# Kernel tuning notes

Hardware: AMD Instinct MI355X
Metric: run time of the kernel (lower is better)

## Reference

```python
import jax, jax.numpy as jnp
import numpy as np

B, S, D = 2048, 8, 1280
K = 1                 # n_components_remove
HIGH_T = 0.6          # PC1_HIGH_ACTIVITY_THRESHOLD
STORM_T = 0.8         # solar_storm_threshold


def setup_inputs() -> dict:
    key = jax.random.key(0)
    k1, k2 = jax.random.split(key, 2)
    features = jax.random.normal(k1, (B, S, D), dtype=jnp.float32)
    kp_index = jax.random.uniform(k2, (B,), dtype=jnp.float32) * 9.0
    cmr_gate = jnp.ones((1,), dtype=jnp.float32)  # nn.Parameter(torch.ones(1))
    return {"features": features, "kp_index": kp_index, "cmr_gate": cmr_gate}


def reference(features, kp_index, cmr_gate):
    # Per-sample standardization over the feature axis (numpy std, ddof=0)
    mu = features.mean(axis=2, keepdims=True)            # (B, S, 1)
    sigma = features.std(axis=2, keepdims=True) + 1e-8   # (B, S, 1)
    fn = (features - mu) / sigma                         # (B, S, D)

    # Batched thin SVD of the (S, D) normalized feature matrix
    U, sv, Vt = jnp.linalg.svd(fn, full_matrices=False)  # (B,S,S), (B,S), (B,S,D)
    var = sv * sv
    pc1_ratio = var[:, 0] / (var.sum(axis=-1) + 1e-8)    # (B,)

    # solar_flag: 0 normal, 1 high activity, 2 storm
    solar_flag = (pc1_ratio >= HIGH_T).astype(jnp.int32) + (pc1_ratio >= STORM_T).astype(jnp.int32)

    # Rank-K reconstruction of the common-mode (solar) component
    low = jnp.einsum('bsk,bk,bkd->bsd', U[:, :, :K], sv[:, :K], Vt[:, :K, :])
    clean = (fn - low) * sigma + mu                      # de-normalized cleaned features

    # Kp-gating: amplify CMR when Kp >= 5
    kp_gate = 1.0 + 0.5 * (kp_index >= 5.0).astype(features.dtype)[:, None, None]
    clean = features + kp_gate * (clean - features)

    # Learnable gate
    gate = jax.nn.sigmoid(cmr_gate)[0]
    features_clean = features + gate * (clean - features)
    return features_clean, pc1_ratio, solar_flag
```

## Files before the change

kernel.cpp:

```cpp
#include <hip/hip_runtime.h>
#include <math.h>


#define SV 8
#define DV 1280
#define D4 320
#define BSTRIDE (SV*DV)
#define LDW 44
#define NP 44
#define WSS 17

__global__ __launch_bounds__(320)
void cmr_gram(const float* __restrict__ feat,
              float* __restrict__ gram)
{
    __shared__ float lds[NP * LDW];
    const int tid  = threadIdx.x;
    const int lane = tid & 63;
    const int wq   = tid >> 6;
    const int b    = blockIdx.x;

    const float4* __restrict__ f4 = (const float4*)(feat + (size_t)b * BSTRIDE);
    const int d4 = wq * 64 + lane;
    float4 f[8];
#pragma unroll
    for (int s = 0; s < 8; ++s) f[s] = f4[s * D4 + d4];

    float Sr[8], C[36];
#pragma unroll
    for (int s = 0; s < 8; ++s) Sr[s] = (f[s].x + f[s].y) + (f[s].z + f[s].w);
    {
        int idx = 0;
#pragma unroll
        for (int i2 = 0; i2 < 8; ++i2)
#pragma unroll
            for (int j2 = i2; j2 < 8; ++j2) {
                float t0 = fmaf(f[i2].x, f[j2].x, fmaf(f[i2].y, f[j2].y, 0.f));
                C[idx] = fmaf(f[i2].z, f[j2].z, fmaf(f[i2].w, f[j2].w, t0));
                ++idx;
            }
    }
#pragma unroll
    for (int m = 1; m <= 4; m <<= 1) {
#pragma unroll
        for (int s = 0; s < 8; ++s) Sr[s] += __shfl_xor(Sr[s], m);
#pragma unroll
        for (int t = 0; t < 36; ++t) C[t] += __shfl_xor(C[t], m);
    }
    {
        const int p = wq * 8 + (lane >> 3);
        if ((lane & 7) == 0) {
#pragma unroll
            for (int t = 0; t < 36; ++t) lds[t * LDW + p] = C[t];
#pragma unroll
            for (int s = 0; s < 8; ++s) lds[(36 + s) * LDW + p] = Sr[s];
        }
    }
    __syncthreads();
    if (wq != 0) return;

    if (lane < NP) {
        const float4* l4 = (const float4*)lds;
        float4 a4 = make_float4(0.f, 0.f, 0.f, 0.f);
#pragma unroll
        for (int q = 0; q < 10; ++q) {
            float4 v = l4[lane * (LDW / 4) + q];
            a4.x += v.x; a4.y += v.y; a4.z += v.z; a4.w += v.w;
        }
        gram[(size_t)b * NP + lane] = (a4.x + a4.y) + (a4.z + a4.w);
    }
}

__global__ __launch_bounds__(256)
void cmr_eigen(const float* __restrict__ gram,
               const float* __restrict__ kp,
               const float* __restrict__ cmr_gate,
               float* __restrict__ coef,
               float* __restrict__ out,
               int Bn)
{
    const int lane = threadIdx.x & 63;
    const int b = blockIdx.x * 4 + (threadIdx.x >> 6);

    const int Lr = (lane < NP) ? lane : 0;
    const float tot = gram[(size_t)b * NP + Lr];

    const int i = lane >> 3, j = lane & 7;
    const int a_ = (i < j) ? i : j;
    const int b_ = (i < j) ? j : i;
    const int tii = 8 * i - (i * (i - 1)) / 2;
    const int tjj = 8 * j - (j * (j - 1)) / 2;
    const int tij = 8 * a_ - (a_ * (a_ - 1)) / 2 + (b_ - a_);
    const float Cij = __shfl(tot, tij);
    const float Ci  = __shfl(tot, tii);
    const float Cj  = __shfl(tot, tjj);
    const float Si  = __shfl(tot, 36 + i);
    const float Sj  = __shfl(tot, 36 + j);

    const float invD = 1.f / (float)DV;
    const float mui = Si * invD, muj = Sj * invD;
    const float vari = fmaxf(Ci * invD - mui * mui, 0.f);
    const float varj = fmaxf(Cj * invD - muj * muj, 0.f);
    const float sigi  = sqrtf(vari) + 1e-8f;
    const float rsigi = 1.f / sigi;
    const float rsigj = 1.f / (sqrtf(varj) + 1e-8f);
    const float G = ((Cij - (float)DV * mui * muj) * rsigi) * rsigj;

    float tr = 0.f;
#pragma unroll
    for (int k = 0; k < 8; ++k) tr += __shfl(G, 9 * k);

    float A = G / fmaxf(tr, 1e-30f);
#pragma unroll
    for (int t = 0; t < 14; ++t) {
        float nb = 0.f;
#pragma unroll
        for (int k = 0; k < 8; ++k)
            nb = fmaf(__shfl(A, i * 8 + k), __shfl(A, k * 8 + j), nb);
        float dg = 0.f;
#pragma unroll
        for (int k = 0; k < 8; ++k) dg += __shfl(nb, 9 * k);
        A = nb / fmaxf(dg, 1e-30f);
    }
    float best = __shfl(A, 0); int bj = 0;
#pragma unroll
    for (int k = 1; k < 8; ++k) {
        float dk = __shfl(A, 9 * k);
        if (dk > best) { best = dk; bj = k; }
    }
    float u = __shfl(A, i * 8 + bj);
    {
        float nn = 0.f;
#pragma unroll
        for (int k = 0; k < 8; ++k) nn += __shfl(u * u, 9 * k);
        u *= rsqrtf(fmaxf(nn, 1e-30f));
    }
#pragma unroll
    for (int it = 0; it < 2; ++it) {
        float y = G * __shfl(u, 9 * j);
#pragma unroll
        for (int m = 1; m <= 4; m <<= 1) y += __shfl_xor(y, m);
        float ny = 0.f;
#pragma unroll
        for (int k = 0; k < 8; ++k) ny += __shfl(y * y, 9 * k);
        u = y * rsqrtf(fmaxf(ny, 1e-30f));
    }
    float v = G * u * __shfl(u, 9 * j);
#pragma unroll
    for (int m = 1; m <= 4; m <<= 1) v += __shfl_xor(v, m);
    float lam = 0.f;
#pragma unroll
    for (int k = 0; k < 8; ++k) lam += __shfl(v, 9 * k);
    const float pc1 = lam / (tr + 1e-8f);

    const float gate = 1.f / (1.f + expf(-cmr_gate[0]));
    const float kpg  = (kp[b] >= 5.0f) ? 1.5f : 1.0f;
    const float Gt   = gate * kpg;

    float bc = 0.f;
#pragma unroll
    for (int k = 0; k < 8; ++k) bc += __shfl(u * rsigi * mui, 9 * k);

    float* wsb = coef + (size_t)b * WSS;
    if (j == 0) {
        wsb[i]     = u * rsigi;
        wsb[8 + i] = Gt * sigi * u;
    }
    if (lane == 0) {
        wsb[16] = bc;
        out[(size_t)Bn * BSTRIDE + b] = pc1;
        const float flag = (pc1 >= 0.6f ? 1.f : 0.f) + (pc1 >= 0.8f ? 1.f : 0.f);
        out[(size_t)Bn * BSTRIDE + Bn + b] = flag;
    }
}

__global__ __launch_bounds__(320)
void cmr_apply(const float* __restrict__ feat,
               const float* __restrict__ coef,
               float* __restrict__ out)
{
    const int tid  = threadIdx.x;
    const int lane = tid & 63;
    const int wq   = tid >> 6;
    const int b    = blockIdx.x;

    const float* __restrict__ wsb = coef + (size_t)b * WSS;
    float a[8], c[8];
#pragma unroll
    for (int s = 0; s < 8; ++s) { a[s] = wsb[s]; c[s] = wsb[8 + s]; }
    const float bc = wsb[16];

    const float4* __restrict__ f4 = (const float4*)(feat + (size_t)b * BSTRIDE);
    float4* __restrict__ o4 = (float4*)(out + (size_t)b * BSTRIDE);
    const int d4 = wq * 64 + lane;

    float4 f[8];
#pragma unroll
    for (int s = 0; s < 8; ++s) f[s] = f4[s * D4 + d4];

    float4 p = make_float4(-bc, -bc, -bc, -bc);
#pragma unroll
    for (int s = 0; s < 8; ++s) {
        p.x = fmaf(a[s], f[s].x, p.x);
        p.y = fmaf(a[s], f[s].y, p.y);
        p.z = fmaf(a[s], f[s].z, p.z);
        p.w = fmaf(a[s], f[s].w, p.w);
    }
#pragma unroll
    for (int s = 0; s < 8; ++s) {
        float4 o;
        o.x = fmaf(-c[s], p.x, f[s].x);
        o.y = fmaf(-c[s], p.y, f[s].y);
        o.z = fmaf(-c[s], p.z, f[s].z);
        o.w = fmaf(-c[s], p.w, f[s].w);
        o4[s * D4 + d4] = o;
    }
}

extern "C" void kernel_launch(void* const* d_in, const int* in_sizes, int n_in,
                              void* d_out, int out_size, void* d_ws, size_t ws_size,
                              hipStream_t stream) {
    const float* feat = (const float*)d_in[0];
    const float* kp   = (const float*)d_in[1];
    const float* gate = (const float*)d_in[2];
    float* out = (float*)d_out;
    const int Bn = in_sizes[0] / BSTRIDE;

    float* gram = (float*)d_ws;
    float* coef = gram + (size_t)Bn * NP;

    cmr_gram <<<Bn,      320, 0, stream>>>(feat, gram);
    cmr_eigen<<<Bn / 4,  256, 0, stream>>>(gram, kp, gate, coef, out, Bn);
    cmr_apply<<<Bn,      320, 0, stream>>>(feat, coef, out);
}
```

Baseline: 178.5 us.

## Compute Gram matrix with bf16 split MFMA and run eigen solve per thread

The Gram/sum reduction now runs on MFMA matrix cores: each fp32 value is split into bf16 hi and lo parts, and hi*hi, hi*lo and sums against a ones vector are accumulated. Each wave handles two batch items. The eigen kernel is reorganized so each thread owns one batch item with the full 8x8 matrix in registers, replacing cross-lane shuffles. It also cuts the squaring iterations from 14 to 12 and uses symmetric products. This trades exact fp32 accumulation for split-bf16 precision (the lo*lo term is dropped) and raises register pressure in the eigen kernel.

Result: faster. 174.5 us (-2.2%).

```diff
diff --git a/kernel.cpp b/kernel.cpp
--- a/kernel.cpp
+++ b/kernel.cpp
@@ -6,72 +6,82 @@
 #define DV 1280
 #define D4 320
 #define BSTRIDE (SV*DV)
-#define LDW 44
-#define NP 44
+#define GSZ 136
 #define WSS 17
 
-__global__ __launch_bounds__(320)
-void cmr_gram(const float* __restrict__ feat,
-              float* __restrict__ gram)
+typedef __attribute__((ext_vector_type(8))) short bf16x8;
+typedef __attribute__((ext_vector_type(4))) float f32x4;
+
+union BF8 { bf16x8 v; short s[8]; };
+
+__device__ __forceinline__ short f2bf(float x) {
+    unsigned u = __float_as_uint(x);
+    return (short)((u + 0x7FFFu + ((u >> 16) & 1u)) >> 16);
+}
+__device__ __forceinline__ float bf2f(short h) {
+    return __uint_as_float(((unsigned)(unsigned short)h) << 16);
+}
+
+__global__ __launch_bounds__(256)
+void cmr_gram(const float* __restrict__ feat, float* __restrict__ gram)
 {
-    __shared__ float lds[NP * LDW];
-    const int tid  = threadIdx.x;
-    const int lane = tid & 63;
-    const int wq   = tid >> 6;
-    const int b    = blockIdx.x;
-
-    const float4* __restrict__ f4 = (const float4*)(feat + (size_t)b * BSTRIDE);
-    const int d4 = wq * 64 + lane;
-    float4 f[8];
-#pragma unroll
-    for (int s = 0; s < 8; ++s) f[s] = f4[s * D4 + d4];
-
-    float Sr[8], C[36];
-#pragma unroll
-    for (int s = 0; s < 8; ++s) Sr[s] = (f[s].x + f[s].y) + (f[s].z + f[s].w);
-    {
-        int idx = 0;
-#pragma unroll
-        for (int i2 = 0; i2 < 8; ++i2)
-#pragma unroll
-            for (int j2 = i2; j2 < 8; ++j2) {
-                float t0 = fmaf(f[i2].x, f[j2].x, fmaf(f[i2].y, f[j2].y, 0.f));
-                C[idx] = fmaf(f[i2].z, f[j2].z, fmaf(f[i2].w, f[j2].w, t0));
-                ++idx;
-            }
-    }
-#pragma unroll
-    for (int m = 1; m <= 4; m <<= 1) {
-#pragma unroll
-        for (int s = 0; s < 8; ++s) Sr[s] += __shfl_xor(Sr[s], m);
-#pragma unroll
-        for (int t = 0; t < 36; ++t) C[t] += __shfl_xor(C[t], m);
-    }
-    {
-        const int p = wq * 8 + (lane >> 3);
-        if ((lane & 7) == 0) {
-#pragma unroll
-            for (int t = 0; t < 36; ++t) lds[t * LDW + p] = C[t];
-#pragma unroll
-            for (int s = 0; s < 8; ++s) lds[(36 + s) * LDW + p] = Sr[s];
-        }
-    }
-    __syncthreads();
-    if (wq != 0) return;
-
-    if (lane < NP) {
-        const float4* l4 = (const float4*)lds;
-        float4 a4 = make_float4(0.f, 0.f, 0.f, 0.f);
-#pragma unroll
-        for (int q = 0; q < 10; ++q) {
-            float4 v = l4[lane * (LDW / 4) + q];
-            a4.x += v.x; a4.y += v.y; a4.z += v.z; a4.w += v.w;
-        }
-        gram[(size_t)b * NP + lane] = (a4.x + a4.y) + (a4.z + a4.w);
-    }
-}
-
-__global__ __launch_bounds__(256)
+    const int lane = threadIdx.x & 63;
+    const int wid  = (blockIdx.x * 256 + threadIdx.x) >> 6;
+    const int m    = lane & 15;
+    const int quad = lane >> 4;
+    const int bt   = m >> 3;
+    const int row  = m & 7;
+
+    const float* __restrict__ fb =
+        feat + ((size_t)(wid * 2 + bt)) * BSTRIDE + (size_t)row * DV;
+
+    BF8 ones;
+#pragma unroll
+    for (int j = 0; j < 8; ++j) ones.s[j] = (short)0x3F80;
+
+    f32x4 accHH = {0.f, 0.f, 0.f, 0.f};
+    f32x4 accHL = {0.f, 0.f, 0.f, 0.f};
+    f32x4 accS  = {0.f, 0.f, 0.f, 0.f};
+
+#pragma unroll 4
+    for (int c = 0; c < 40; ++c) {
+        const int k0 = c * 32 + quad * 8;
+        const float4 x0 = *(const float4*)(fb + k0);
+        const float4 x1 = *(const float4*)(fb + k0 + 4);
+        float x[8] = {x0.x, x0.y, x0.z, x0.w, x1.x, x1.y, x1.z, x1.w};
+        BF8 hi, lo;
+#pragma unroll
+        for (int j = 0; j < 8; ++j) {
+            hi.s[j] = f2bf(x[j]);
+            lo.s[j] = f2bf(x[j] - bf2f(hi.s[j]));
+        }
+        accHH = __builtin_amdgcn_mfma_f32_16x16x32_bf16(hi.v, hi.v,   accHH, 0, 0, 0);
+        accHL = __builtin_amdgcn_mfma_f32_16x16x32_bf16(hi.v, lo.v,   accHL, 0, 0, 0);
+        accS  = __builtin_amdgcn_mfma_f32_16x16x32_bf16(hi.v, ones.v, accS,  0, 0, 0);
+        accS  = __builtin_amdgcn_mfma_f32_16x16x32_bf16(lo.v, ones.v, accS,  0, 0, 0);
+    }
+
+    const int colb = (lane & 15) >> 3;
+    const int col  = lane & 7;
+#pragma unroll
+    for (int r = 0; r < 4; ++r) {
+        const int rowg = quad * 4 + r;
+        if ((rowg >> 3) == colb) {
+            float* gb = gram + ((size_t)(wid * 2 + colb)) * GSZ;
+            gb[(rowg & 7) * 8 + col]      = accHH[r];
+            gb[64 + (rowg & 7) * 8 + col] = accHL[r];
+        }
+    }
+    if ((lane & 15) == 0) {
+#pragma unroll
+        for (int r = 0; r < 4; ++r) {
+            const int rowg = quad * 4 + r;
+            gram[((size_t)(wid * 2 + (rowg >> 3))) * GSZ + 128 + (rowg & 7)] = accS[r];
+        }
+    }
+}
+
+__global__ __launch_bounds__(64, 1)
 void cmr_eigen(const float* __restrict__ gram,
                const float* __restrict__ kp,
                const float* __restrict__ cmr_gate,
@@ -79,78 +89,109 @@
                float* __restrict__ out,
                int Bn)
 {
-    const int lane = threadIdx.x & 63;
-    const int b = blockIdx.x * 4 + (threadIdx.x >> 6);
-
-    const int Lr = (lane < NP) ? lane : 0;
-    const float tot = gram[(size_t)b * NP + Lr];
-
-    const int i = lane >> 3, j = lane & 7;
-    const int a_ = (i < j) ? i : j;
-    const int b_ = (i < j) ? j : i;
-    const int tii = 8 * i - (i * (i - 1)) / 2;
-    const int tjj = 8 * j - (j * (j - 1)) / 2;
-    const int tij = 8 * a_ - (a_ * (a_ - 1)) / 2 + (b_ - a_);
-    const float Cij = __shfl(tot, tij);
-    const float Ci  = __shfl(tot, tii);
-    const float Cj  = __shfl(tot, tjj);
-    const float Si  = __shfl(tot, 36 + i);
-    const float Sj  = __shfl(tot, 36 + j);
-
+    const int b = blockIdx.x * 64 + threadIdx.x;
+    const float* __restrict__ g = gram + (size_t)b * GSZ;
+
+    float G[8][8], S[8], mu[8], sig[8], rsig[8];
+#pragma unroll
+    for (int i = 0; i < 8; ++i) {
+#pragma unroll
+        for (int j = 0; j < 8; ++j)
+            G[i][j] = g[i * 8 + j] + g[64 + i * 8 + j] + g[64 + j * 8 + i];
+        S[i] = g[128 + i];
+    }
     const float invD = 1.f / (float)DV;
-    const float mui = Si * invD, muj = Sj * invD;
-    const float vari = fmaxf(Ci * invD - mui * mui, 0.f);
-    const float varj = fmaxf(Cj * invD - muj * muj, 0.f);
-    const float sigi  = sqrtf(vari) + 1e-8f;
-    const float rsigi = 1.f / sigi;
-    const float rsigj = 1.f / (sqrtf(varj) + 1e-8f);
-    const float G = ((Cij - (float)DV * mui * muj) * rsigi) * rsigj;
+#pragma unroll
+    for (int i = 0; i < 8; ++i) {
+        mu[i] = S[i] * invD;
+        const float var = fmaxf(G[i][i] * invD - mu[i] * mu[i], 0.f);
+        sig[i]  = sqrtf(var) + 1e-8f;
+        rsig[i] = 1.f / sig[i];
+    }
+#pragma unroll
+    for (int i = 0; i < 8; ++i)
+#pragma unroll
+        for (int j = 0; j < 8; ++j)
+            G[i][j] = (G[i][j] - (float)DV * mu[i] * mu[j]) * rsig[i] * rsig[j];
 
     float tr = 0.f;
 #pragma unroll
-    for (int k = 0; k < 8; ++k) tr += __shfl(G, 9 * k);
-
-    float A = G / fmaxf(tr, 1e-30f);
-#pragma unroll
-    for (int t = 0; t < 14; ++t) {
-        float nb = 0.f;
-#pragma unroll
-        for (int k = 0; k < 8; ++k)
-            nb = fmaf(__shfl(A, i * 8 + k), __shfl(A, k * 8 + j), nb);
-        float dg = 0.f;
-#pragma unroll
-        for (int k = 0; k < 8; ++k) dg += __shfl(nb, 9 * k);
-        A = nb / fmaxf(dg, 1e-30f);
-    }
-    float best = __shfl(A, 0); int bj = 0;
-#pragma unroll
-    for (int k = 1; k < 8; ++k) {
-        float dk = __shfl(A, 9 * k);
-        if (dk > best) { best = dk; bj = k; }
-    }
-    float u = __shfl(A, i * 8 + bj);
+    for (int i = 0; i < 8; ++i) tr += G[i][i];
+
+    float A[8][8];
+    {
+        const float rt = 1.f / fmaxf(tr, 1e-30f);
+#pragma unroll
+        for (int i = 0; i < 8; ++i)
+#pragma unroll
+            for (int j = 0; j < 8; ++j) A[i][j] = G[i][j] * rt;
+    }
+#pragma unroll
+    for (int t = 0; t < 12; ++t) {
+        float Bm[8][8];
+        float trB = 0.f;
+#pragma unroll
+        for (int i = 0; i < 8; ++i)
+#pragma unroll
+            for (int j = i; j < 8; ++j) {
+                float acc = 0.f;
+#pragma unroll
+                for (int k = 0; k < 8; ++k)
+                    acc = fmaf(A[i][k], A[j][k], acc);
+                Bm[i][j] = acc;
+                if (i == j) trB += acc;
+            }
+        const float rt = 1.f / fmaxf(trB, 1e-30f);
+#pragma unroll
+        for (int i = 0; i < 8; ++i)
+#pragma unroll
+            for (int j = i; j < 8; ++j) {
+                const float v = Bm[i][j] * rt;
+                A[i][j] = v; A[j][i] = v;
+            }
+    }
+    int bj = 0; float best = A[0][0];
+#pragma unroll
+    for (int k = 1; k < 8; ++k)
+        if (A[k][k] > best) { best = A[k][k]; bj = k; }
+    float u[8];
+#pragma unroll
+    for (int i = 0; i < 8; ++i) {
+        float v = A[i][0];
+#pragma unroll
+        for (int k = 1; k < 8; ++k) v = (bj == k) ? A[i][k] : v;
+        u[i] = v;
+    }
     {
         float nn = 0.f;
 #pragma unroll
-        for (int k = 0; k < 8; ++k) nn += __shfl(u * u, 9 * k);
-        u *= rsqrtf(fmaxf(nn, 1e-30f));
+        for (int i = 0; i < 8; ++i) nn = fmaf(u[i], u[i], nn);
+        const float r = rsqrtf(fmaxf(nn, 1e-30f));
+#pragma unroll
+        for (int i = 0; i < 8; ++i) u[i] *= r;
     }
 #pragma unroll
     for (int it = 0; it < 2; ++it) {
-        float y = G * __shfl(u, 9 * j);
-#pragma unroll
-        for (int m = 1; m <= 4; m <<= 1) y += __shfl_xor(y, m);
-        float ny = 0.f;
-#pragma unroll
-        for (int k = 0; k < 8; ++k) ny += __shfl(y * y, 9 * k);
-        u = y * rsqrtf(fmaxf(ny, 1e-30f));
-    }
-    float v = G * u * __shfl(u, 9 * j);
-#pragma unroll
-    for (int m = 1; m <= 4; m <<= 1) v += __shfl_xor(v, m);
+        float y[8]; float ny = 0.f;
+#pragma unroll
+        for (int i = 0; i < 8; ++i) {
+            float acc = 0.f;
+#pragma unroll
+            for (int k = 0; k < 8; ++k) acc = fmaf(G[i][k], u[k], acc);
+            y[i] = acc; ny = fmaf(acc, acc, ny);
+        }
+        const float r = rsqrtf(fmaxf(ny, 1e-30f));
+#pragma unroll
+        for (int i = 0; i < 8; ++i) u[i] = y[i] * r;
+    }
     float lam = 0.f;
 #pragma unroll
-    for (int k = 0; k < 8; ++k) lam += __shfl(v, 9 * k);
+    for (int i = 0; i < 8; ++i) {
+        float acc = 0.f;
+#pragma unroll
+        for (int k = 0; k < 8; ++k) acc = fmaf(G[i][k], u[k], acc);
+        lam = fmaf(u[i], acc, lam);
+    }
     const float pc1 = lam / (tr + 1e-8f);
 
     const float gate = 1.f / (1.f + expf(-cmr_gate[0]));
@@ -159,19 +200,18 @@
 
     float bc = 0.f;
 #pragma unroll
-    for (int k = 0; k < 8; ++k) bc += __shfl(u * rsigi * mui, 9 * k);
+    for (int i = 0; i < 8; ++i) bc = fmaf(u[i] * rsig[i], mu[i], bc);
 
     float* wsb = coef + (size_t)b * WSS;
-    if (j == 0) {
-        wsb[i]     = u * rsigi;
-        wsb[8 + i] = Gt * sigi * u;
-    }
-    if (lane == 0) {
-        wsb[16] = bc;
-        out[(size_t)Bn * BSTRIDE + b] = pc1;
-        const float flag = (pc1 >= 0.6f ? 1.f : 0.f) + (pc1 >= 0.8f ? 1.f : 0.f);
-        out[(size_t)Bn * BSTRIDE + Bn + b] = flag;
-    }
+#pragma unroll
+    for (int i = 0; i < 8; ++i) {
+        wsb[i]     = u[i] * rsig[i];
+        wsb[8 + i] = Gt * sig[i] * u[i];
+    }
+    wsb[16] = bc;
+    out[(size_t)Bn * BSTRIDE + b] = pc1;
+    out[(size_t)Bn * BSTRIDE + Bn + b] =
+        (pc1 >= 0.6f ? 1.f : 0.f) + (pc1 >= 0.8f ? 1.f : 0.f);
 }
 
 __global__ __launch_bounds__(320)
@@ -227,9 +267,9 @@
     const int Bn = in_sizes[0] / BSTRIDE;
 
     float* gram = (float*)d_ws;
-    float* coef = gram + (size_t)Bn * NP;
-
-    cmr_gram <<<Bn,      320, 0, stream>>>(feat, gram);
-    cmr_eigen<<<Bn / 4,  256, 0, stream>>>(gram, kp, gate, coef, out, Bn);
+    float* coef = gram + (size_t)Bn * GSZ;
+
+    cmr_gram <<<Bn / 8,  256, 0, stream>>>(feat, gram);
+    cmr_eigen<<<Bn / 64, 64,  0, stream>>>(gram, kp, gate, coef, out, Bn);
     cmr_apply<<<Bn,      320, 0, stream>>>(feat, coef, out);
 }
```
